# Optimization experiments

Hardware: AMD Instinct MI355X
Metric: run time of the kernel (lower is better)

The kernel has to match this reference:

```python
import jax, jax.numpy as jnp
import numpy as np

B, FRAMES, NBINS, HOP = 4, 400, 129, 240
T = FRAMES * HOP  # 96000


def hann_window(K, dtype=jnp.float32):
    # torch.hann_window default is periodic=True: 0.5*(1 - cos(2*pi*n/K))
    n = jnp.arange(K, dtype=dtype)
    return 0.5 - 0.5 * jnp.cos(2.0 * jnp.pi * n / K)


def get_minimum_phase_fir(log_mag):
    # log_mag: [B, F, NBINS] -> full spectrum [B, F, N], N = 2*(NBINS-1)
    full = jnp.concatenate([log_mag, jnp.flip(log_mag, -1)[..., 1:-1]], axis=-1)
    N = full.shape[-1]
    # Hilbert transform (scipy-style analytic signal), N even
    Xf = jnp.fft.fft(full, axis=-1)
    h = jnp.concatenate([
        jnp.ones((1,), full.dtype),
        2.0 * jnp.ones((N // 2 - 1,), full.dtype),
        jnp.ones((1,), full.dtype),
        jnp.zeros((N // 2 - 1,), full.dtype),
    ])
    analytic = jnp.fft.ifft(Xf * h, axis=-1)
    min_phase = -jnp.imag(analytic)
    freq_resp = jnp.exp(full + 1j * min_phase)
    return jnp.real(jnp.fft.ifft(freq_resp, axis=-1))  # [B, F, N]


def windowing(kernel):
    K = kernel.shape[-1]
    w = hann_window(K, kernel.dtype)
    w = w.at[: K // 2].set(1.0)
    return kernel * w


def upsample_linear(x, scale):
    # x: [B, K, L] -> [B, K, L*scale], matches F.upsample(mode='linear', align_corners=False)
    L = x.shape[-1]
    out = jnp.arange(L * scale, dtype=x.dtype)
    src = jnp.clip((out + 0.5) / scale - 0.5, 0.0, L - 1.0)
    lo = jnp.floor(src).astype(jnp.int32)
    hi = jnp.minimum(lo + 1, L - 1)
    w = src - lo.astype(x.dtype)
    return x[..., lo] * (1.0 - w) + x[..., hi] * w


def fir_filt(x, h):
    # x: [B, T], h: [B, T, K]; causal time-varying FIR: y[t] = sum_k h[t,k] * x[t-k]
    K = h.shape[-1]
    Tn = x.shape[-1]
    x_pad = jnp.pad(x, ((0, 0), (K - 1, 0)))
    idx = jnp.arange(Tn)[:, None] + jnp.arange(K)[None, :]  # [T, K]
    frames = x_pad[:, idx]  # [B, T, K] (im2col-like gather)
    return jnp.einsum('btk,btk->bt', frames, jnp.flip(h, -1))


def setup_inputs() -> dict:
    key = jax.random.key(0)
    k1, k2 = jax.random.split(key)
    ex = jax.random.normal(k1, (B, T), dtype=jnp.float32)
    log_mag = jax.random.normal(k2, (B, FRAMES, NBINS), dtype=jnp.float32)
    return {"ex": ex, "log_mag": log_mag, "hop_length": HOP}


def reference(ex, log_mag, hop_length):
    kernel = get_minimum_phase_fir(log_mag)          # [B, F, K]
    kernel = windowing(kernel)
    up = upsample_linear(jnp.transpose(kernel, (0, 2, 1)), hop_length)  # [B, K, F*hop]
    up = jnp.transpose(up, (0, 2, 1))                # [B, F*hop, K]
    Tn = min(ex.shape[1], up.shape[1])
    ex = ex[:, :Tn]
    up = up[:, :Tn]
    return fir_filt(ex, up)
```

## Files before the change

### kernel.cpp

```cpp
#include <hip/hip_runtime.h>
#include <math.h>

#define NB 4
#define FRAMES 400
#define NBINS 129
#define HOP 240
#define T_LEN (FRAMES * HOP)
#define KLEN 256

#define REC_C { const float cn_ = fmaf(a2, cm, -cm1); cm1 = cm; cm = cn_; }
#define REC_S { const float sn_ = fmaf(a2, sm, -sm1); sm1 = sm; sm = sn_; }

__global__ __launch_bounds__(128) void gen_fir(const float* __restrict__ log_mag,
                                               float* __restrict__ kern) {
    const int bf = blockIdx.x;
    const int n  = threadIdx.x;

    __shared__ __align__(16) float  full[132];
    __shared__ __align__(16) float  g[128];
    __shared__ __align__(16) float2 crci[128];

    const float* lm = log_mag + bf * NBINS;
    full[n] = lm[n];
    if (n == 0) full[128] = lm[128];

    const float rev_n = (float)n * (1.0f / 256.0f);
    const float ca = __builtin_amdgcn_cosf(rev_n);
    const float sa = __builtin_amdgcn_sinf(rev_n);
    const float a2  = 2.0f * ca;
    const float sgn = (n & 1) ? -1.0f : 1.0f;
    __syncthreads();

    const float full0   = full[0];
    const float full128 = full[128];

    {
        const float4* f4p = (const float4*)full;
        float cm1 = ca, cm = 1.0f, acc = 0.0f;
#pragma unroll 8
        for (int u = 0; u < 32; ++u) {
            const float4 f4 = f4p[u];
            acc = fmaf(f4.x, cm, acc); REC_C;
            acc = fmaf(f4.y, cm, acc); REC_C;
            acc = fmaf(f4.z, cm, acc); REC_C;
            acc = fmaf(f4.w, cm, acc); REC_C;
        }
        const float Xf = 2.0f * acc - full0 + sgn * full128;
        g[n] = Xf * (1.0f / 128.0f);
    }
    __syncthreads();

    {
        const float4* g4p = (const float4*)g;
        float sm1 = -sa, sm = 0.0f, acc = 0.0f;
#pragma unroll 8
        for (int u = 0; u < 32; ++u) {
            const float4 gv = g4p[u];
            acc = fmaf(gv.x, sm, acc); REC_S;
            acc = fmaf(gv.y, sm, acc); REC_S;
            acc = fmaf(gv.z, sm, acc); REC_S;
            acc = fmaf(gv.w, sm, acc); REC_S;
        }
        const float mp = -acc;
        const float e  = __builtin_amdgcn_exp2f(full[n] * 1.4426950408889634f);
        float rev = mp * 0.15915494309189535f;
        rev = rev - floorf(rev);
        const float smp  = __builtin_amdgcn_sinf(rev);
        const float cmp_ = __builtin_amdgcn_cosf(rev);
        const float sc = (n == 0) ? 1.0f : 2.0f;
        crci[n] = make_float2(sc * e * cmp_, sc * e * smp);
    }
    __syncthreads();

    {
        const float e128 = __builtin_amdgcn_exp2f(full128 * 1.4426950408889634f);
        const float4* cc4 = (const float4*)crci;
        float cm1 = ca, cm = 1.0f;
        float sm1 = -sa, sm = 0.0f;
        float accE = 0.0f, accO = 0.0f;
#pragma unroll 8
        for (int u = 0; u < 64; ++u) {
            const float4 q = cc4[u];
            accE = fmaf(q.x, cm, accE); accE = fmaf(-q.y, sm, accE);
            REC_C; REC_S;
            accO = fmaf(q.z, cm, accO); accO = fmaf(-q.w, sm, accO);
            REC_C; REC_S;
        }
        const float base = sgn * e128;
        const float s = 1.0f / 256.0f;
        kern[bf * KLEN + n]       = (accE + accO + base) * s;
        kern[bf * KLEN + n + 128] = (accE - accO + base) * s * (0.5f + 0.5f * ca);
    }
}

__global__ __launch_bounds__(256) void fir_apply(const float* __restrict__ ex,
                                                 const float* __restrict__ kern,
                                                 float* __restrict__ out) {
    const int b   = blockIdx.y;
    const int t0  = blockIdx.x * 512;
    const int tid = threadIdx.x;

    __shared__ __align__(16) float  xs[768];
    __shared__ __align__(16) float2 kp[4][258];

    for (int i = tid; i < 768; i += 256) {
        const int t = t0 - 255 + i;
        xs[i] = (t >= 0 && t < T_LEN) ? ex[b * T_LEN + t] : 0.0f;
    }

    float src0 = ((float)t0 + 0.5f) * (1.0f / HOP) - 0.5f;
    src0 = fminf(fmaxf(src0, 0.0f), (float)(FRAMES - 1));
    const int f0 = (int)src0;
    const float* kb = kern + b * FRAMES * KLEN;
    for (int i = tid; i < 4 * KLEN; i += 256) {
        const int q = i >> 8;
        const int j = i & 255;
        const int fl = min(f0 + q,     FRAMES - 1);
        const int fh = min(f0 + q + 1, FRAMES - 1);
        kp[q][j] = make_float2(kb[fl * KLEN + j], kb[fh * KLEN + j]);
    }
    __syncthreads();

    const int te = t0 + 2 * tid;
    float se = ((float)te + 0.5f) * (1.0f / HOP) - 0.5f;
    se = fminf(fmaxf(se, 0.0f), (float)(FRAMES - 1));
    float so = ((float)te + 1.5f) * (1.0f / HOP) - 0.5f;
    so = fminf(fmaxf(so, 0.0f), (float)(FRAMES - 1));
    const int   lo = (int)se;
    const float we = se - (float)lo;
    const float wo = so - (float)lo;

    const float4* kq4 = (const float4*)&kp[lo - f0][0];

    const int base = 2 * tid;
    float carry = xs[base + 256];
    float aeL = 0.0f, aeH = 0.0f, aoL = 0.0f, aoH = 0.0f;
#pragma unroll 8
    for (int u = 0; u < 128; ++u) {
        const float2 v  = *(const float2*)&xs[base + 254 - 2 * u];
        const float4 k4 = kq4[u];
        aeL = fmaf(v.y,   k4.x, aeL);  aeH = fmaf(v.y,   k4.y, aeH);
        aoL = fmaf(carry, k4.x, aoL);  aoH = fmaf(carry, k4.y, aoH);
        aeL = fmaf(v.x,   k4.z, aeL);  aeH = fmaf(v.x,   k4.w, aeH);
        aoL = fmaf(v.y,   k4.z, aoL);  aoH = fmaf(v.y,   k4.w, aoH);
        carry = v.x;
    }

    if (te < T_LEN)     out[b * T_LEN + te]     = (1.0f - we) * aeL + we * aeH;
    if (te + 1 < T_LEN) out[b * T_LEN + te + 1] = (1.0f - wo) * aoL + wo * aoH;
}

extern "C" void kernel_launch(void* const* d_in, const int* in_sizes, int n_in,
                              void* d_out, int out_size, void* d_ws, size_t ws_size,
                              hipStream_t stream) {
    const float* ex      = (const float*)d_in[0];
    const float* log_mag = (const float*)d_in[1];
    float* kern = (float*)d_ws;
    float* out  = (float*)d_out;

    gen_fir<<<NB * FRAMES, 128, 0, stream>>>(log_mag, kern);

    dim3 grid((T_LEN + 511) / 512, NB);
    fir_apply<<<grid, 256, 0, stream>>>(ex, kern, out);
}
```

Measured before the change: 24.34 us.

## Register-block four outputs per thread pair and split taps across two lanes

Each pair of threads now computes four consecutive outputs, with each lane handling half of the 256 taps. The halves are combined with a lane shuffle and written as one float4 store. Loading each excitation sample once as a float4 and reusing it for four outputs is meant to cut LDS reads per FMA. Costs are the extra shuffles, more accumulator registers, and an assumption that four consecutive outputs share the same frame index lo. If a HOP boundary falls inside a group of four, that assumption could be wrong.

Measured after the change: 27.31 us. +12.2%, slower.

```diff
diff --git a/kernel.cpp b/kernel.cpp
--- a/kernel.cpp
+++ b/kernel.cpp
@@ -99,12 +99,14 @@
     const int b   = blockIdx.y;
     const int t0  = blockIdx.x * 512;
     const int tid = threadIdx.x;
+    const int g   = tid >> 1;
+    const int h   = tid & 1;
 
     __shared__ __align__(16) float  xs[768];
     __shared__ __align__(16) float2 kp[4][258];
 
     for (int i = tid; i < 768; i += 256) {
-        const int t = t0 - 255 + i;
+        const int t = t0 - 256 + i;
         xs[i] = (t >= 0 && t < T_LEN) ? ex[b * T_LEN + t] : 0.0f;
     }
 
@@ -121,33 +123,65 @@
     }
     __syncthreads();
 
-    const int te = t0 + 2 * tid;
-    float se = ((float)te + 0.5f) * (1.0f / HOP) - 0.5f;
-    se = fminf(fmaxf(se, 0.0f), (float)(FRAMES - 1));
-    float so = ((float)te + 1.5f) * (1.0f / HOP) - 0.5f;
-    so = fminf(fmaxf(so, 0.0f), (float)(FRAMES - 1));
-    const int   lo = (int)se;
-    const float we = se - (float)lo;
-    const float wo = so - (float)lo;
+    const int te0 = t0 + 4 * g;
+    if (te0 >= T_LEN) return;
+
+    float s0 = ((float)te0 + 0.5f) * (1.0f / HOP) - 0.5f;
+    s0 = fminf(fmaxf(s0, 0.0f), (float)(FRAMES - 1));
+    const int lo = (int)s0;
+    float w[4];
+#pragma unroll
+    for (int r = 0; r < 4; ++r) {
+        float sr = ((float)(te0 + r) + 0.5f) * (1.0f / HOP) - 0.5f;
+        sr = fminf(fmaxf(sr, 0.0f), (float)(FRAMES - 1));
+        w[r] = sr - (float)lo;
+    }
 
     const float4* kq4 = (const float4*)&kp[lo - f0][0];
+    const float4* xs4 = (const float4*)xs;
 
-    const int base = 2 * tid;
-    float carry = xs[base + 256];
-    float aeL = 0.0f, aeH = 0.0f, aoL = 0.0f, aoH = 0.0f;
-#pragma unroll 8
-    for (int u = 0; u < 128; ++u) {
-        const float2 v  = *(const float2*)&xs[base + 254 - 2 * u];
-        const float4 k4 = kq4[u];
-        aeL = fmaf(v.y,   k4.x, aeL);  aeH = fmaf(v.y,   k4.y, aeH);
-        aoL = fmaf(carry, k4.x, aoL);  aoH = fmaf(carry, k4.y, aoH);
-        aeL = fmaf(v.x,   k4.z, aeL);  aeH = fmaf(v.x,   k4.w, aeH);
-        aoL = fmaf(v.y,   k4.z, aoL);  aoH = fmaf(v.y,   k4.w, aoH);
-        carry = v.x;
+    float aL0 = 0, aL1 = 0, aL2 = 0, aL3 = 0;
+    float aH0 = 0, aH1 = 0, aH2 = 0, aH3 = 0;
+
+    float4 Rp = xs4[g + 64 - 32 * h];
+    const int kbase = 64 * h;
+#pragma unroll 4
+    for (int u = 0; u < 32; ++u) {
+        const float4 Rc = xs4[g + 63 - 32 * h - u];
+        const float4 ka = kq4[kbase + 2 * u];
+        const float4 kb4 = kq4[kbase + 2 * u + 1];
+        aL0 = fmaf(Rp.x, ka.x, aL0); aH0 = fmaf(Rp.x, ka.y, aH0);
+        aL1 = fmaf(Rp.y, ka.x, aL1); aH1 = fmaf(Rp.y, ka.y, aH1);
+        aL2 = fmaf(Rp.z, ka.x, aL2); aH2 = fmaf(Rp.z, ka.y, aH2);
+        aL3 = fmaf(Rp.w, ka.x, aL3); aH3 = fmaf(Rp.w, ka.y, aH3);
+        aL0 = fmaf(Rc.w, ka.z, aL0); aH0 = fmaf(Rc.w, ka.w, aH0);
+        aL1 = fmaf(Rp.x, ka.z, aL1); aH1 = fmaf(Rp.x, ka.w, aH1);
+        aL2 = fmaf(Rp.y, ka.z, aL2); aH2 = fmaf(Rp.y, ka.w, aH2);
+        aL3 = fmaf(Rp.z, ka.z, aL3); aH3 = fmaf(Rp.z, ka.w, aH3);
+        aL0 = fmaf(Rc.z, kb4.x, aL0); aH0 = fmaf(Rc.z, kb4.y, aH0);
+        aL1 = fmaf(Rc.w, kb4.x, aL1); aH1 = fmaf(Rc.w, kb4.y, aH1);
+        aL2 = fmaf(Rp.x, kb4.x, aL2); aH2 = fmaf(Rp.x, kb4.y, aH2);
+        aL3 = fmaf(Rp.y, kb4.x, aL3); aH3 = fmaf(Rp.y, kb4.y, aH3);
+        aL0 = fmaf(Rc.y, kb4.z, aL0); aH0 = fmaf(Rc.y, kb4.w, aH0);
+        aL1 = fmaf(Rc.z, kb4.z, aL1); aH1 = fmaf(Rc.z, kb4.w, aH1);
+        aL2 = fmaf(Rc.w, kb4.z, aL2); aH2 = fmaf(Rc.w, kb4.w, aH2);
+        aL3 = fmaf(Rp.x, kb4.z, aL3); aH3 = fmaf(Rp.x, kb4.w, aH3);
+        Rp = Rc;
     }
 
-    if (te < T_LEN)     out[b * T_LEN + te]     = (1.0f - we) * aeL + we * aeH;
-    if (te + 1 < T_LEN) out[b * T_LEN + te + 1] = (1.0f - wo) * aoL + wo * aoH;
+    aL0 += __shfl_xor(aL0, 1); aH0 += __shfl_xor(aH0, 1);
+    aL1 += __shfl_xor(aL1, 1); aH1 += __shfl_xor(aH1, 1);
+    aL2 += __shfl_xor(aL2, 1); aH2 += __shfl_xor(aH2, 1);
+    aL3 += __shfl_xor(aL3, 1); aH3 += __shfl_xor(aH3, 1);
+
+    if (h == 0) {
+        float4 y;
+        y.x = aL0 + w[0] * (aH0 - aL0);
+        y.y = aL1 + w[1] * (aH1 - aL1);
+        y.z = aL2 + w[2] * (aH2 - aL2);
+        y.w = aL3 + w[3] * (aH3 - aL3);
+        *(float4*)(out + b * T_LEN + te0) = y;
+    }
 }
 
 extern "C" void kernel_launch(void* const* d_in, const int* in_sizes, int n_in,
```

## Split gen_fir DFT reductions across two thread halves per frame

Applied to the files above, without the earlier changes.

gen_fir now launches 256 threads per frame instead of 128. Each half computes half of every DFT summation, seeding the Chebyshev cosine/sine recurrence at the half's start index, and the partial sums are combined through shared memory. The goal is to halve the serial recurrence chain per thread and raise occupancy for the 1600-block launch. In exchange it adds extra barriers and shared-memory reductions, and the second half's recurrence starts from a different seed, which changes rounding slightly.

Result: no change. 24.31 us (median of 2 runs) (-0.1%).

```diff
diff --git a/kernel.cpp b/kernel.cpp
--- a/kernel.cpp
+++ b/kernel.cpp
@@ -11,24 +11,41 @@
 #define REC_C { const float cn_ = fmaf(a2, cm, -cm1); cm1 = cm; cm = cn_; }
 #define REC_S { const float sn_ = fmaf(a2, sm, -sm1); sm1 = sm; sm = sn_; }
 
-__global__ __launch_bounds__(128) void gen_fir(const float* __restrict__ log_mag,
+__global__ __launch_bounds__(256) void gen_fir(const float* __restrict__ log_mag,
                                                float* __restrict__ kern) {
-    const int bf = blockIdx.x;
-    const int n  = threadIdx.x;
+    const int bf  = blockIdx.x;
+    const int tid = threadIdx.x;
+    const int n   = tid & 127;
+    const int h   = tid >> 7;
 
     __shared__ __align__(16) float  full[132];
-    __shared__ __align__(16) float  g[128];
+    __shared__ __align__(16) float  pg[2][128];
+    __shared__ __align__(16) float  pm[2][128];
     __shared__ __align__(16) float2 crci[128];
+    __shared__ __align__(16) float  pe[2][128];
+    __shared__ __align__(16) float  po[2][128];
 
     const float* lm = log_mag + bf * NBINS;
-    full[n] = lm[n];
-    if (n == 0) full[128] = lm[128];
+    if (tid < NBINS) full[tid] = lm[tid];
 
     const float rev_n = (float)n * (1.0f / 256.0f);
     const float ca = __builtin_amdgcn_cosf(rev_n);
     const float sa = __builtin_amdgcn_sinf(rev_n);
     const float a2  = 2.0f * ca;
     const float sgn = (n & 1) ? -1.0f : 1.0f;
+
+    float cm0, cm1_0, sm0, sm1_0;
+    if (h == 0) {
+        cm0 = 1.0f;  cm1_0 = ca;
+        sm0 = 0.0f;  sm1_0 = -sa;
+    } else {
+        const float r64 = (float)((64 * n) & 255) * (1.0f / 256.0f);
+        const float r63 = (float)((63 * n) & 255) * (1.0f / 256.0f);
+        cm0   = __builtin_amdgcn_cosf(r64);
+        sm0   = __builtin_amdgcn_sinf(r64);
+        cm1_0 = __builtin_amdgcn_cosf(r63);
+        sm1_0 = __builtin_amdgcn_sinf(r63);
+    }
     __syncthreads();
 
     const float full0   = full[0];
@@ -36,32 +53,39 @@
 
     {
         const float4* f4p = (const float4*)full;
-        float cm1 = ca, cm = 1.0f, acc = 0.0f;
+        float cm1 = cm1_0, cm = cm0, acc = 0.0f;
 #pragma unroll 8
-        for (int u = 0; u < 32; ++u) {
+        for (int u = 16 * h; u < 16 * h + 16; ++u) {
             const float4 f4 = f4p[u];
             acc = fmaf(f4.x, cm, acc); REC_C;
             acc = fmaf(f4.y, cm, acc); REC_C;
             acc = fmaf(f4.z, cm, acc); REC_C;
             acc = fmaf(f4.w, cm, acc); REC_C;
         }
-        const float Xf = 2.0f * acc - full0 + sgn * full128;
-        g[n] = Xf * (1.0f / 128.0f);
+        const float share = h ? (sgn * full128) : (-full0);
+        pg[h][n] = acc * (1.0f / 64.0f) + share * (1.0f / 128.0f);
     }
     __syncthreads();
 
     {
-        const float4* g4p = (const float4*)g;
-        float sm1 = -sa, sm = 0.0f, acc = 0.0f;
+        const float4* p0 = (const float4*)pg[0];
+        const float4* p1 = (const float4*)pg[1];
+        float sm1 = sm1_0, sm = sm0, acc = 0.0f;
 #pragma unroll 8
-        for (int u = 0; u < 32; ++u) {
-            const float4 gv = g4p[u];
-            acc = fmaf(gv.x, sm, acc); REC_S;
-            acc = fmaf(gv.y, sm, acc); REC_S;
-            acc = fmaf(gv.z, sm, acc); REC_S;
-            acc = fmaf(gv.w, sm, acc); REC_S;
+        for (int u = 16 * h; u < 16 * h + 16; ++u) {
+            const float4 a4 = p0[u];
+            const float4 b4 = p1[u];
+            acc = fmaf(a4.x + b4.x, sm, acc); REC_S;
+            acc = fmaf(a4.y + b4.y, sm, acc); REC_S;
+            acc = fmaf(a4.z + b4.z, sm, acc); REC_S;
+            acc = fmaf(a4.w + b4.w, sm, acc); REC_S;
         }
-        const float mp = -acc;
+        pm[h][n] = acc;
+    }
+    __syncthreads();
+
+    if (h == 0) {
+        const float mp = -(pm[0][n] + pm[1][n]);
         const float e  = __builtin_amdgcn_exp2f(full[n] * 1.4426950408889634f);
         float rev = mp * 0.15915494309189535f;
         rev = rev - floorf(rev);
@@ -73,19 +97,27 @@
     __syncthreads();
 
     {
-        const float e128 = __builtin_amdgcn_exp2f(full128 * 1.4426950408889634f);
         const float4* cc4 = (const float4*)crci;
-        float cm1 = ca, cm = 1.0f;
-        float sm1 = -sa, sm = 0.0f;
+        float cm1 = cm1_0, cm = cm0;
+        float sm1 = sm1_0, sm = sm0;
         float accE = 0.0f, accO = 0.0f;
 #pragma unroll 8
-        for (int u = 0; u < 64; ++u) {
+        for (int u = 32 * h; u < 32 * h + 32; ++u) {
             const float4 q = cc4[u];
             accE = fmaf(q.x, cm, accE); accE = fmaf(-q.y, sm, accE);
             REC_C; REC_S;
             accO = fmaf(q.z, cm, accO); accO = fmaf(-q.w, sm, accO);
             REC_C; REC_S;
         }
+        pe[h][n] = accE;
+        po[h][n] = accO;
+    }
+    __syncthreads();
+
+    if (h == 0) {
+        const float accE = pe[0][n] + pe[1][n];
+        const float accO = po[0][n] + po[1][n];
+        const float e128 = __builtin_amdgcn_exp2f(full128 * 1.4426950408889634f);
         const float base = sgn * e128;
         const float s = 1.0f / 256.0f;
         kern[bf * KLEN + n]       = (accE + accO + base) * s;
@@ -158,7 +190,7 @@
     float* kern = (float*)d_ws;
     float* out  = (float*)d_out;
 
-    gen_fir<<<NB * FRAMES, 128, 0, stream>>>(log_mag, kern);
+    gen_fir<<<NB * FRAMES, 256, 0, stream>>>(log_mag, kern);
 
     dim3 grid((T_LEN + 511) / 512, NB);
     fir_apply<<<grid, 256, 0, stream>>>(ex, kern, out);
```
